# Performance work log

Hardware: AMD Instinct MI355X
Metric: run time of the kernel (lower is better)

The kernel has to match this reference:

```python
import jax, jax.numpy as jnp
import numpy as np

NUM_NODES = 10000
D = 128      # input_dim (embedding dim)
N = 64       # visit_code_num
V = 50       # visit_thresh (time steps)
B = 256      # batch
H = 384      # hidden_dim
L = 8        # levels
CH = H // L  # chunk_size
K = 10       # conv_size (sliding window / conv kernel)
OUT = 128    # output_dim
ND = N * D


def setup_inputs() -> dict:
    key = jax.random.key(0)
    ks = jax.random.split(key, 16)
    node_ids = jax.random.randint(ks[0], (B, V, N), 0, NUM_NODES + 1)
    edge_idx = jax.random.randint(ks[1], (2, 4), 0, 100)
    edge_attr = jax.random.normal(ks[2], (4, 1), jnp.float32)
    visit_times = jax.random.uniform(ks[3], (B, V), jnp.float32)
    visit_order = jax.random.randint(ks[4], (B, V), 0, V)
    attn_mask = jnp.zeros((B, V, N), dtype=bool)
    embed = jax.random.normal(ks[5], (NUM_NODES + 1, D), jnp.float32) * 0.02
    embed = embed.at[0].set(0.0)  # padding_idx=0
    G = 4 * H + 2 * L
    Wk = jax.random.normal(ks[6], (G, ND + 1), jnp.float32) * 0.01
    bk = jnp.zeros((G,), jnp.float32)
    Wr = jax.random.normal(ks[7], (G, H + 1), jnp.float32) * 0.05
    br = jnp.zeros((G,), jnp.float32)
    Ws = jax.random.normal(ks[8], (H // 6, H), jnp.float32) * 0.05
    bs = jnp.zeros((H // 6,), jnp.float32)
    Wrs = jax.random.normal(ks[9], (H, H // 6), jnp.float32) * 0.05
    brs = jnp.zeros((H,), jnp.float32)
    Wc = jax.random.normal(ks[10], (H, H, K), jnp.float32) * 0.02  # Conv1d weight [out,in,k]
    bc = jnp.zeros((H,), jnp.float32)
    Wo = jax.random.normal(ks[11], (OUT, H), jnp.float32) * 0.05
    bo = jnp.zeros((OUT,), jnp.float32)
    return dict(node_ids=node_ids, edge_idx=edge_idx, edge_attr=edge_attr,
                visit_times=visit_times, visit_order=visit_order, attn_mask=attn_mask,
                embed=embed, Wk=Wk, bk=bk, Wr=Wr, br=br, Ws=Ws, bs=bs,
                Wrs=Wrs, brs=brs, Wc=Wc, bc=bc, Wo=Wo, bo=bo)


def _cumax_l2r(z):
    return jnp.cumsum(jax.nn.softmax(z, -1), -1)


def _cumax_r2l(z):
    s = jax.nn.softmax(z, -1)
    return jnp.flip(jnp.cumsum(jnp.flip(s, -1), -1), -1)


def _forward(node_ids, attn_mask, visit_times, embed, Wk, bk, Wr, br,
             Ws, bs, Wrs, brs, Wc, bc, Wo, bo):
    b, v, n = node_ids.shape
    # gather(expand(embed), node_ids) == plain embedding lookup
    x = embed[node_ids].reshape(b, v, n * D)  # [B,V,ND]

    def step(carry, xt):
        c, h, tmp_h, tmp_dis = carry
        inp, interval = xt
        xi = jnp.concatenate([inp, interval[:, None]], -1)   # [B,ND+1]
        hi = jnp.concatenate([h, interval[:, None]], -1)     # [B,H+1]
        xout = xi @ Wk.T + bk + hi @ Wr.T + br               # [B,4H+2L]
        fm = _cumax_l2r(xout[:, :L])[:, :, None]             # [B,L,1]
        im = _cumax_r2l(xout[:, L:2 * L])[:, :, None]        # [B,L,1]
        g = xout[:, 2 * L:].reshape(b, 4 * L, CH)
        f = jax.nn.sigmoid(g[:, :L])
        i = jax.nn.sigmoid(g[:, L:2 * L])
        o = jax.nn.sigmoid(g[:, 2 * L:3 * L])
        cin = jnp.tanh(g[:, 3 * L:])
        cl = c.reshape(b, L, CH)
        ov = fm * im
        c_new = ov * (f * cl + i * cin) + (fm - ov) * cl + (im - ov) * cin
        h_new = (o * jnp.tanh(c_new)).reshape(b, H)
        c_new = c_new.reshape(b, H)
        cur_dist = 1.0 - jnp.mean(fm[:, :, 0], -1)           # [B]
        tmp_h = jnp.concatenate([tmp_h[1:], h_new[None]], 0)        # [K,B,H]
        tmp_dis = jnp.concatenate([tmp_dis[1:], cur_dist[None]], 0)  # [K,B]
        local_dis = jax.nn.softmax(jnp.cumsum(tmp_dis.T, 1), 1)     # [B,K]
        local_h = tmp_h.transpose(1, 2, 0) * local_dis[:, None, :]  # [B,H,K]
        theme = jnp.mean(local_h, -1)                               # [B,H]
        theme = jax.nn.sigmoid(jax.nn.relu(theme @ Ws.T + bs) @ Wrs.T + brs)
        conv = jnp.einsum('bhk,ohk->bo', local_h, Wc) + bc          # Conv1d, out len 1
        return (c_new, h_new, tmp_h, tmp_dis), (h_new, theme * conv)

    carry0 = (jnp.zeros((b, H), x.dtype), jnp.zeros((b, H), x.dtype),
              jnp.zeros((K, b, H), x.dtype), jnp.zeros((K, b), x.dtype))
    _, (origin_h, hs) = jax.lax.scan(step, carry0,
                                     (x.transpose(1, 0, 2), visit_times.T))
    rnn = (hs + origin_h).transpose(1, 0, 2)   # [B,V,H]
    output = rnn @ Wo.T + bo                   # [B,V,OUT]
    visit_mask = jnp.all(attn_mask, -1)        # [B,V] True = padded visit
    last = jnp.sum((~visit_mask).astype(jnp.int32), -1) - 1
    return output[jnp.arange(b), last]         # [B,OUT] logits


def reference(node_ids, edge_idx, edge_attr, visit_times, visit_order, attn_mask,
              embed, Wk, bk, Wr, br, Ws, bs, Wrs, brs, Wc, bc, Wo, bo):
    return _forward(node_ids, attn_mask, visit_times, embed, Wk, bk, Wr, br,
                    Ws, bs, Wrs, brs, Wc, bc, Wo, bo)
```

## Files before the change

kernel.cpp:

```cpp
#include <hip/hip_runtime.h>
#include <stdint.h>


typedef unsigned short u16;
typedef short bf16x8 __attribute__((ext_vector_type(8)));
typedef float f32x4 __attribute__((ext_vector_type(4)));

#define GLL(gp, lp)                                                            \
  __builtin_amdgcn_global_load_lds(                                            \
      (const __attribute__((address_space(1))) unsigned int*)(gp),             \
      (__attribute__((address_space(3))) unsigned int*)(lp), 16, 0, 0)

__device__ __forceinline__ float bf2f(u16 u) {
  union { unsigned int i; float f; } v;
  v.i = ((unsigned int)u) << 16;
  return v.f;
}
__device__ __forceinline__ u16 f2bf(float f) {
  union { float f; unsigned int i; } v;
  v.f = f;
  unsigned int r = (v.i + 0x7fffu + ((v.i >> 16) & 1u)) >> 16;
  return (u16)r;
}
__device__ __forceinline__ float ldf(const void* p, size_t i, int isbf) {
  return isbf ? bf2f(((const u16*)p)[i]) : ((const float*)p)[i];
}
__device__ __forceinline__ float sigf(float x) { return 1.f / (1.f + __expf(-x)); }
__device__ __forceinline__ float tanhf_(float x) {
  float cx = fminf(fmaxf(x, -15.f), 15.f);
  float e = __expf(2.f * cx);
  return (e - 1.f) / (e + 1.f);
}
__device__ __forceinline__ float dot8_bf(const u16* w, const float* lp) {
  uint4 wv = *(const uint4*)w;
  union { unsigned int u; float f; } a0, a1;
  float s;
  a0.u = wv.x << 16; a1.u = wv.x & 0xffff0000u;
  s = lp[0] * a0.f + lp[1] * a1.f;
  a0.u = wv.y << 16; a1.u = wv.y & 0xffff0000u;
  s += lp[2] * a0.f + lp[3] * a1.f;
  a0.u = wv.z << 16; a1.u = wv.z & 0xffff0000u;
  s += lp[4] * a0.f + lp[5] * a1.f;
  a0.u = wv.w << 16; a1.u = wv.w & 0xffff0000u;
  s += lp[6] * a0.f + lp[7] * a1.f;
  return s;
}

__device__ __forceinline__ int gperm(int gp) {
  if (gp < 16) return gp;
  int r = gp - 16;
  int q = r & 3, h = r >> 2;
  return 16 + q * 384 + h;
}

__global__ void k_detect(const unsigned int* __restrict__ emb_raw,
                         int* __restrict__ flag) {
  if (blockIdx.x == 0 && threadIdx.x == 0) {
    int cnt = 0;
    for (int i = 64; i < 128; ++i) {
      unsigned int u = emb_raw[i];
      unsigned int lo = u & 0xffffu;
      unsigned int ex = (lo >> 7) & 0xffu;
      if (lo != 0 && ex >= 100 && ex <= 126) ++cnt;
    }
    *flag = (cnt >= 32) ? 1 : 0;
  }
}

__global__ void k_cvt_emb(const void* __restrict__ src, u16* __restrict__ dst,
                          const int* __restrict__ flagp) {
  int isbf = *flagp;
  int n = 10001 * 128;
  int i = blockIdx.x * blockDim.x + threadIdx.x;
  int stride = gridDim.x * blockDim.x;
  for (; i < n; i += stride)
    dst[i] = isbf ? ((const u16*)src)[i] : f2bf(((const float*)src)[i]);
}

__global__ void k_repack_wk(const void* __restrict__ wk, u16* __restrict__ wkp,
                            const int* __restrict__ flagp) {
  int isbf = *flagp;
  size_t i = (size_t)blockIdx.x * blockDim.x + threadIdx.x;
  size_t total = (size_t)1664 * 8192;
  size_t stride = (size_t)gridDim.x * blockDim.x;
  for (; i < total; i += stride) {
    size_t gp = i >> 13, k = i & 8191;
    u16 v = (u16)0;
    if (gp < 1552) {
      int g = gperm((int)gp);
      v = f2bf(ldf(wk, (size_t)g * 8193 + k, isbf));
    }
    wkp[i] = v;
  }
}

__global__ void k_prep_wr2(const void* __restrict__ wr, const void* __restrict__ wk,
                           const void* __restrict__ bk, const void* __restrict__ br,
                           u16* __restrict__ wrP2, float* __restrict__ biasC,
                           float* __restrict__ wlC, const int* __restrict__ flagp) {
  int isbf = *flagp;
  int i0 = blockIdx.x * blockDim.x + threadIdx.x;
  int stride = gridDim.x * blockDim.x;
  for (int j = i0; j < 1552 * 384; j += stride) {
    int gp = j / 384, k = j - gp * 384;
    int g = gperm(gp);
    wrP2[j] = f2bf(ldf(wr, (size_t)g * 385 + k, isbf));
  }
  for (int gp = i0; gp < 1552; gp += stride) {
    int g = gperm(gp);
    biasC[gp] = ldf(bk, g, isbf) + ldf(br, g, isbf);
    wlC[gp] = ldf(wk, (size_t)g * 8193 + 8192, isbf) + ldf(wr, g * 385 + 384, isbf);
  }
}

__global__ void k_repack_wc(const void* __restrict__ wc, u16* __restrict__ wcp,
                            const int* __restrict__ flagp) {
  int isbf = *flagp;
  int i0 = blockIdx.x * blockDim.x + threadIdx.x;
  int stride = gridDim.x * blockDim.x;
  for (int j = i0; j < 384 * 3840; j += stride) {
    int o = j / 3840;
    int r = j - o * 3840;
    int k = r / 384;
    int h = r - k * 384;
    wcp[j] = f2bf(ldf(wc, (o * 384 + h) * 10 + k, isbf));
  }
}

__global__ void k_cvt_smalls(const void* vt, const void* Ws, const void* bs,
                             const void* Wrs, const void* brs, const void* bc,
                             const void* Wo, const void* bo,
                             float* __restrict__ dst, const int* __restrict__ flagp) {
  int isbf = *flagp;
  int i = blockIdx.x * blockDim.x + threadIdx.x;
  int stride = gridDim.x * blockDim.x;
  for (; i < 112064; i += stride) {
    float v;
    if (i < 12800) v = ldf(vt, i, isbf);
    else if (i < 37376) v = ldf(Ws, i - 12800, isbf);
    else if (i < 37440) v = ldf(bs, i - 37376, isbf);
    else if (i < 62016) v = ldf(Wrs, i - 37440, isbf);
    else if (i < 62400) v = ldf(brs, i - 62016, isbf);
    else if (i < 62784) v = ldf(bc, i - 62400, isbf);
    else if (i < 111936) v = ldf(Wo, i - 62784, isbf);
    else v = ldf(bo, i - 111936, isbf);
    dst[i] = v;
  }
}

__global__ void k_zero(float* __restrict__ p, int n) {
  int i = blockIdx.x * blockDim.x + threadIdx.x;
  int stride = gridDim.x * blockDim.x;
  for (; i < n; i += stride) p[i] = 0.f;
}

__global__ __launch_bounds__(256) void k_gemm_xk(
    const int* __restrict__ node_ids, const u16* __restrict__ embB,
    const u16* __restrict__ wkp, const float* __restrict__ vtF,
    const float* __restrict__ biasC, const float* __restrict__ wlC,
    u16* __restrict__ xkb) {
  __shared__ alignas(16) u16 As[128 * 64];
  __shared__ alignas(16) u16 Bs[128 * 64];
  __shared__ alignas(16) u16 idS[128 * 64];
  int tid = threadIdx.x;
  int lin = blockIdx.x;
  int xcd = lin & 7, slot = lin >> 3;
  int job = (xcd < 4) ? (xcd * 163 + slot) : (4 * 163 + (xcd - 4) * 162 + slot);
  int mb = job % 100, gb = job / 100;
  int m0 = mb * 128;
  int g0 = gb * 128;
  int tq = m0 >> 8, b0t = m0 & 255;
  int lane = tid & 63, w = tid >> 6;
  int wy = w >> 1, wx = w & 1;
  f32x4 acc[4][4];
#pragma unroll
  for (int i = 0; i < 4; ++i)
#pragma unroll
    for (int j = 0; j < 4; ++j) acc[i][j] = (f32x4){0.f, 0.f, 0.f, 0.f};

  {
    const int4* nb = (const int4*)(node_ids + ((size_t)b0t * 50 + tq) * 64);
    for (int i = tid; i < 2048; i += 256) {
      int row = i >> 4, c4 = i & 15;
      int4 v = nb[(size_t)row * 800 + c4];
      u16* d = idS + row * 64 + c4 * 4;
      d[0] = (u16)v.x; d[1] = (u16)v.y; d[2] = (u16)v.z; d[3] = (u16)v.w;
    }
  }

  int l15 = lane & 15, lq = lane >> 4;
  int lr = lane >> 3, lc = lane & 7;
  int swc = (lc ^ lr) * 8;
  int cRd = (lq ^ (l15 & 7)) * 8;

  for (int kt = 0; kt < 128; ++kt) {
    __syncthreads();
#pragma unroll
    for (int c = 0; c < 4; ++c) {
      int chunk = w * 4 + c;
      int r = chunk * 8 + lr;
      int id = (int)idS[r * 64 + (kt >> 1)];
      const u16* gp = embB + (size_t)id * 128 + (kt & 1) * 64 + swc;
      u16* lp = As + chunk * 512 + lane * 8;
      GLL(gp, lp);
    }
#pragma unroll
    for (int c = 0; c < 4; ++c) {
      int chunk = w * 4 + c;
      int r = chunk * 8 + lr;
      const u16* gp = wkp + (size_t)(g0 + r) * 8192 + (size_t)kt * 64 + swc;
      u16* lp = Bs + chunk * 512 + lane * 8;
      GLL(gp, lp);
    }
    __syncthreads();
    const u16* Ab = As + (wy * 64 + l15) * 64;
    const u16* Bb = Bs + (wx * 64 + l15) * 64;
#pragma unroll
    for (int ks = 0; ks < 2; ++ks) {
      int co = cRd ^ (ks * 32);
      bf16x8 av[4], bv[4];
#pragma unroll
      for (int i = 0; i < 4; ++i) av[i] = *(const bf16x8*)(Ab + i * 1024 + co);
#pragma unroll
      for (int j = 0; j < 4; ++j) bv[j] = *(const bf16x8*)(Bb + j * 1024 + co);
#pragma unroll
      for (int i = 0; i < 4; ++i)
#pragma unroll
        for (int j = 0; j < 4; ++j)
          acc[i][j] =
              __builtin_amdgcn_mfma_f32_16x16x32_bf16(av[i], bv[j], acc[i][j], 0, 0, 0);
    }
  }
  float vt[4][4];
#pragma unroll
  for (int i = 0; i < 4; ++i)
#pragma unroll
    for (int p = 0; p < 4; ++p)
      vt[i][p] = vtF[(size_t)(b0t + wy * 64 + i * 16 + lq * 4 + p) * 50 + tq];
#pragma unroll
  for (int j = 0; j < 4; ++j) {
    int gcol = g0 + wx * 64 + j * 16 + l15;
    if (gcol < 1552) {
      float bC = biasC[gcol], wC = wlC[gcol];
#pragma unroll
      for (int i = 0; i < 4; ++i)
#pragma unroll
        for (int p = 0; p < 4; ++p) {
          int row = wy * 64 + i * 16 + lq * 4 + p;
          xkb[(size_t)(m0 + row) * 1552 + gcol] =
              f2bf(acc[i][j][p] + bC + vt[i][p] * wC);
        }
    }
  }
}

__global__ __launch_bounds__(512) void k_step2(
    const u16* __restrict__ xkb,
    const u16* __restrict__ wrP2,
    float* __restrict__ hbuf,
    float* __restrict__ dbuf,
    const u16* __restrict__ hin,
    u16* __restrict__ hout,
    float* __restrict__ cst,
    int t) {
  __shared__ alignas(16) u16 hS[16 * 400];
  __shared__ alignas(16) float fmTile[16 * 17];
  __shared__ float fmS[16][8], imS[16][8];
  int tid = threadIdx.x;
  int gs = blockIdx.x, b0 = blockIdx.y * 16;
  int wv = tid >> 6, lane = tid & 63, l15 = lane & 15, lq = lane >> 4;

  int hmy = gs * 32 + wv * 4 + lq;
  int bmy = b0 + l15;

  uint2 xkg = *(const uint2*)(xkb + ((size_t)t * 256 + bmy) * 1552 + 16 +
                              gs * 128 + wv * 16 + lq * 4);
  uint4 xksm = (uint4){0u, 0u, 0u, 0u};
  if (tid < 32)
    xksm = *(const uint4*)(xkb + ((size_t)t * 256 + b0 + (tid & 15)) * 1552 +
                           ((tid < 16) ? 0 : 8));
  float cv = cst[(size_t)bmy * 384 + hmy];

  {
    const u16* hsrc = hin + (size_t)b0 * 384;
    for (int idx = tid; idx < 768; idx += 512) {
      int r = idx / 48, c = idx - r * 48;
      *(uint4*)(hS + r * 400 + c * 8) = *(const uint4*)(hsrc + r * 384 + c * 8);
    }
  }
  __syncthreads();

  bf16x8 hb[12];
#pragma unroll
  for (int ks = 0; ks < 12; ++ks)
    hb[ks] = *(const bf16x8*)(hS + l15 * 400 + ks * 32 + lq * 8);

  int gRow = 16 + gs * 128 + wv * 16 + l15;
  const u16* arow = wrP2 + (size_t)gRow * 384 + lq * 8;
  const u16* arow0 = wrP2 + (size_t)l15 * 384 + lq * 8;
  f32x4 accg = (f32x4){0.f, 0.f, 0.f, 0.f};
  f32x4 accf = (f32x4){0.f, 0.f, 0.f, 0.f};
#pragma unroll
  for (int ks = 0; ks < 12; ++ks) {
    bf16x8 ag = *(const bf16x8*)(arow + ks * 32);
    accg = __builtin_amdgcn_mfma_f32_16x16x32_bf16(ag, hb[ks], accg, 0, 0, 0);
    if (wv == 0) {
      bf16x8 a0 = *(const bf16x8*)(arow0 + ks * 32);
      accf = __builtin_amdgcn_mfma_f32_16x16x32_bf16(a0, hb[ks], accf, 0, 0, 0);
    }
  }
  if (wv == 0) {
#pragma unroll
    for (int p = 0; p < 4; ++p) fmTile[(lq * 4 + p) * 17 + l15] = accf[p];
  }
  __syncthreads();

  if (tid < 32) {
    int r = tid & 15;
    const u16* xs = (const u16*)&xksm;
    float z[8], m = -1e30f;
#pragma unroll
    for (int j = 0; j < 8; ++j) {
      int jj = (tid < 16) ? j : (8 + j);
      z[j] = fmTile[jj * 17 + r] + bf2f(xs[j]);
      m = fmaxf(m, z[j]);
    }
    float s = 0.f;
#pragma unroll
    for (int j = 0; j < 8; ++j) { z[j] = __expf(z[j] - m); s += z[j]; }
    float inv = 1.f / s;
    if (tid < 16) {
      float run = 0.f, fsum = 0.f;
#pragma unroll
      for (int j = 0; j < 8; ++j) { run += z[j] * inv; fmS[r][j] = run; fsum += run; }
      if (gs == 0) dbuf[(size_t)t * 256 + b0 + r] = 1.f - fsum * 0.125f;
    } else {
      float run = 0.f;
#pragma unroll
      for (int j = 7; j >= 0; --j) { run += z[j] * inv; imS[r][j] = run; }
    }
  }
  __syncthreads();

  {
    int lmy = hmy / 48;
    const u16* xg = (const u16*)&xkg;
    float x0 = accg[0] + bf2f(xg[0]);
    float x1 = accg[1] + bf2f(xg[1]);
    float x2 = accg[2] + bf2f(xg[2]);
    float x3 = accg[3] + bf2f(xg[3]);
    float fg = sigf(x0), ig = sigf(x1), og = sigf(x2), ci = tanhf_(x3);
    float fm = fmS[l15][lmy], im = imS[l15][lmy];
    float ov = fm * im;
    float cn = ov * (fg * cv + ig * ci) + (fm - ov) * cv + (im - ov) * ci;
    float hn = og * tanhf_(cn);
    cst[(size_t)bmy * 384 + hmy] = cn;
    hbuf[((size_t)t * 256 + bmy) * 384 + hmy] = hn;
    hout[(size_t)bmy * 384 + hmy] = f2bf(hn);
  }
}

__global__ __launch_bounds__(384) void k_final(
    const float* __restrict__ hbuf, const float* __restrict__ dbuf,
    const unsigned char* __restrict__ am, const float* __restrict__ smalls,
    const u16* __restrict__ wcp, float* __restrict__ out) {
  const float* WsF = smalls + 12800;
  const float* bsF = smalls + 37376;
  const float* WrsF = smalls + 37440;
  const float* brsF = smalls + 62016;
  const float* bcF = smalls + 62400;
  const float* WoF = smalls + 62784;
  const float* boF = smalls + 111936;
  __shared__ alignas(16) float lh2[10][384];
  __shared__ alignas(16) float ti[384];
  __shared__ alignas(16) float us[64];
  __shared__ alignas(16) float rnnS[384];
  __shared__ alignas(16) float hlastS[384];
  __shared__ float ldS[10];
  __shared__ int npad[50];
  __shared__ int lastS;
  int tid = threadIdx.x;
  int b = blockIdx.x;

  if (tid < 50) {
    const unsigned char* mr = am + ((size_t)b * 50 + tid) * 64;
    int all1 = 1;
    for (int q = 0; q < 64; ++q) all1 &= (mr[q] != 0);
    npad[tid] = all1 ? 0 : 1;
  }
  __syncthreads();
  if (tid == 0) {
    int c = 0;
    for (int v = 0; v < 50; ++v) c += npad[v];
    int lv = c - 1;
    int last = lv < 0 ? 0 : lv;
    lastS = last;
    float cum = 0.f, cv[10];
    for (int k = 0; k < 10; ++k) {
      int s = last - 9 + k;
      float dk = (s >= 0) ? dbuf[(size_t)s * 256 + b] : 0.f;
      cum += dk;
      cv[k] = cum;
    }
    float m = cv[0];
    for (int k = 1; k < 10; ++k) m = fmaxf(m, cv[k]);
    float ssum = 0.f, ee[10];
    for (int k = 0; k < 10; ++k) { ee[k] = __expf(cv[k] - m); ssum += ee[k]; }
    float inv = 1.f / ssum;
    for (int k = 0; k < 10; ++k) ldS[k] = ee[k] * inv;
  }
  __syncthreads();
  {
    int h = tid;
    int last = lastS;
    float ssum = 0.f;
    for (int k = 0; k < 10; ++k) {
      int s = last - 9 + k;
      float hv = (s >= 0) ? hbuf[((size_t)s * 256 + b) * 384 + h] : 0.f;
      float v = hv * ldS[k];
      lh2[k][h] = v;
      ssum += v;
    }
    ti[h] = ssum * 0.1f;
    hlastS[h] = hbuf[((size_t)last * 256 + b) * 384 + h];
  }
  __syncthreads();
  if (tid < 64) {
    float a = bsF[tid];
    const float* wr = WsF + (size_t)tid * 384;
    for (int h = 0; h < 384; ++h) a += wr[h] * ti[h];
    us[tid] = fmaxf(a, 0.f);
  }
  __syncthreads();
  {
    int o = tid;
    float th = brsF[o];
    const float* wr = WrsF + (size_t)o * 64;
    for (int k = 0; k < 64; ++k) th += wr[k] * us[k];
    th = sigf(th);
    float cacc = bcF[o];
    for (int k = 0; k < 10; ++k) {
      const u16* wrow = wcp + ((size_t)o * 10 + k) * 384;
      const float* lrow = lh2[k];
      for (int h8 = 0; h8 < 48; ++h8) cacc += dot8_bf(wrow + h8 * 8, lrow + h8 * 8);
    }
    rnnS[o] = th * cacc + hlastS[o];
  }
  __syncthreads();
  if (tid < 128) {
    float a = boF[tid];
    const float* wr = WoF + (size_t)tid * 384;
    for (int h = 0; h < 384; ++h) a += wr[h] * rnnS[h];
    out[(size_t)b * 128 + tid] = a;
  }
}

extern "C" void kernel_launch(void* const* d_in, const int* in_sizes, int n_in,
                              void* d_out, int out_size, void* d_ws, size_t ws_size,
                              hipStream_t stream) {
  const int* node_ids = (const int*)d_in[0];
  const void* vtR = d_in[3];
  const unsigned char* am = (const unsigned char*)d_in[5];
  const void* embR = d_in[6];
  const void* WkR = d_in[7];
  const void* bkR = d_in[8];
  const void* WrR = d_in[9];
  const void* brR = d_in[10];
  const void* WsR = d_in[11];
  const void* bsR = d_in[12];
  const void* WrsR = d_in[13];
  const void* brsR = d_in[14];
  const void* WcR = d_in[15];
  const void* bcR = d_in[16];
  const void* WoR = d_in[17];
  const void* boR = d_in[18];
  (void)in_sizes; (void)n_in; (void)out_size; (void)ws_size;

  char* ws = (char*)d_ws;
  size_t off = 0;
  auto alloc = [&](size_t bytes) {
    void* p = ws + off;
    off = (off + bytes + 255) & ~(size_t)255;
    return p;
  };
  int* flagp = (int*)alloc(4);
  u16* embB = (u16*)alloc((size_t)10001 * 128 * 2);
  u16* WkP = (u16*)alloc((size_t)1664 * 8192 * 2);
  u16* WrP2 = (u16*)alloc((size_t)1552 * 384 * 2);
  float* biasC = (float*)alloc(1552 * 4);
  float* wlC = (float*)alloc(1552 * 4);
  float* smalls = (float*)alloc((size_t)112064 * 4);
  u16* XKb = (u16*)alloc((size_t)12800 * 1552 * 2);
  u16* WcP = (u16*)alloc((size_t)384 * 3840 * 2);
  float* Hbuf = (float*)alloc((size_t)50 * 256 * 384 * 4);
  float* Dbuf = (float*)alloc((size_t)50 * 256 * 4);
  u16* Hx = (u16*)alloc((size_t)2 * 256 * 384 * 2);
  float* Cst = (float*)alloc((size_t)256 * 384 * 4);

  k_detect<<<dim3(1), dim3(64), 0, stream>>>((const unsigned int*)embR, flagp);
  k_cvt_emb<<<dim3(1024), dim3(256), 0, stream>>>(embR, embB, flagp);
  k_repack_wk<<<dim3(2048), dim3(256), 0, stream>>>(WkR, WkP, flagp);
  k_prep_wr2<<<dim3(512), dim3(256), 0, stream>>>(WrR, WkR, bkR, brR, WrP2, biasC,
                                                  wlC, flagp);
  k_repack_wc<<<dim3(512), dim3(256), 0, stream>>>(WcR, WcP, flagp);
  k_cvt_smalls<<<dim3(128), dim3(256), 0, stream>>>(vtR, WsR, bsR, WrsR, brsR,
                                                    bcR, WoR, boR, smalls, flagp);
  k_zero<<<dim3(96), dim3(256), 0, stream>>>((float*)Hx, 98304);
  k_zero<<<dim3(96), dim3(256), 0, stream>>>(Cst, 98304);

  k_gemm_xk<<<dim3(1300), dim3(256), 0, stream>>>(node_ids, embB, WkP, smalls,
                                                  biasC, wlC, XKb);

  for (int t = 0; t < 50; ++t) {
    const u16* hin = Hx + (size_t)(t & 1) * (256 * 384);
    u16* hout = Hx + (size_t)((t + 1) & 1) * (256 * 384);
    k_step2<<<dim3(12, 16), dim3(512), 0, stream>>>(XKb, WrP2, Hbuf, Dbuf, hin,
                                                    hout, Cst, t);
  }

  k_final<<<dim3(256), dim3(384), 0, stream>>>(Hbuf, Dbuf, am, smalls, WcP,
                                               (float*)d_out);
}
```

Before: 1.128 ms.

## Fuse 50 recurrent step launches into one persistent kernel with per-group barriers

Replaces 50 separate per-timestep launches with a single persistent kernel of 192 blocks. Each block keeps its recurrent weight slice in LDS and its cell state in registers. Blocks exchange bf16 hidden state through global memory and sync per batch group with an atomic counter spin barrier. This removes launch overhead and repeated weight and cell-state reloads, but relies on all 192 blocks being co-resident and on relaxed atomics for visibility. It also pads the id tile in shared memory to reduce bank conflicts in the gather GEMM.

Measured after the change: 993.2 us. -11.9%, faster.

```diff
diff --git a/kernel.cpp b/kernel.cpp
--- a/kernel.cpp
+++ b/kernel.cpp
@@ -161,7 +161,7 @@
     u16* __restrict__ xkb) {
   __shared__ alignas(16) u16 As[128 * 64];
   __shared__ alignas(16) u16 Bs[128 * 64];
-  __shared__ alignas(16) u16 idS[128 * 64];
+  __shared__ alignas(16) u16 idS[128 * 66];
   int tid = threadIdx.x;
   int lin = blockIdx.x;
   int xcd = lin & 7, slot = lin >> 3;
@@ -183,7 +183,7 @@
     for (int i = tid; i < 2048; i += 256) {
       int row = i >> 4, c4 = i & 15;
       int4 v = nb[(size_t)row * 800 + c4];
-      u16* d = idS + row * 64 + c4 * 4;
+      u16* d = idS + row * 66 + c4 * 4;
       d[0] = (u16)v.x; d[1] = (u16)v.y; d[2] = (u16)v.z; d[3] = (u16)v.w;
     }
   }
@@ -199,7 +199,7 @@
     for (int c = 0; c < 4; ++c) {
       int chunk = w * 4 + c;
       int r = chunk * 8 + lr;
-      int id = (int)idS[r * 64 + (kt >> 1)];
+      int id = (int)idS[r * 66 + (kt >> 1)];
       const u16* gp = embB + (size_t)id * 128 + (kt & 1) * 64 + swc;
       u16* lp = As + chunk * 512 + lane * 8;
       GLL(gp, lp);
@@ -254,109 +254,153 @@
   }
 }
 
-__global__ __launch_bounds__(512) void k_step2(
+__global__ __launch_bounds__(512) void k_scan5(
     const u16* __restrict__ xkb,
     const u16* __restrict__ wrP2,
     float* __restrict__ hbuf,
     float* __restrict__ dbuf,
-    const u16* __restrict__ hin,
-    u16* __restrict__ hout,
-    float* __restrict__ cst,
-    int t) {
-  __shared__ alignas(16) u16 hS[16 * 400];
+    unsigned int* __restrict__ hx,
+    int* __restrict__ barCnt) {
+  __shared__ alignas(16) u16 WrS[144 * 392];
+  __shared__ alignas(16) u16 hS[16 * 392];
   __shared__ alignas(16) float fmTile[16 * 17];
   __shared__ float fmS[16][8], imS[16][8];
+
   int tid = threadIdx.x;
-  int gs = blockIdx.x, b0 = blockIdx.y * 16;
+  int L = blockIdx.x;
+  int xcd = L & 7, kk = L >> 3;
+  int hi = (kk >= 12) ? 1 : 0;
+  int bg = (xcd << 1) | hi;
+  int gs = kk - 12 * hi;
+  int b0 = bg * 16;
   int wv = tid >> 6, lane = tid & 63, l15 = lane & 15, lq = lane >> 4;
 
+  for (int idx = tid; idx < 144 * 48; idx += 512) {
+    int r = idx / 48, c = idx - r * 48;
+    int gr = (r < 16) ? r : (16 + gs * 128 + (r - 16));
+    *(uint4*)(WrS + r * 392 + c * 8) =
+        *(const uint4*)(wrP2 + (size_t)gr * 384 + c * 8);
+  }
+
   int hmy = gs * 32 + wv * 4 + lq;
+  int lmy = hmy / 48;
   int bmy = b0 + l15;
-
-  uint2 xkg = *(const uint2*)(xkb + ((size_t)t * 256 + bmy) * 1552 + 16 +
-                              gs * 128 + wv * 16 + lq * 4);
-  uint4 xksm = (uint4){0u, 0u, 0u, 0u};
-  if (tid < 32)
-    xksm = *(const uint4*)(xkb + ((size_t)t * 256 + b0 + (tid & 15)) * 1552 +
-                           ((tid < 16) ? 0 : 8));
-  float cv = cst[(size_t)bmy * 384 + hmy];
-
-  {
-    const u16* hsrc = hin + (size_t)b0 * 384;
-    for (int idx = tid; idx < 768; idx += 512) {
-      int r = idx / 48, c = idx - r * 48;
-      *(uint4*)(hS + r * 400 + c * 8) = *(const uint4*)(hsrc + r * 384 + c * 8);
-    }
-  }
+  float creg = 0.f;
+
+  const u16* arow_g = WrS + (16 + wv * 16 + l15) * 392 + lq * 8;
+  const u16* arow_f = WrS + l15 * 392 + lq * 8;
+  const u16* brow = hS + l15 * 392 + lq * 8;
   __syncthreads();
 
-  bf16x8 hb[12];
-#pragma unroll
-  for (int ks = 0; ks < 12; ++ks)
-    hb[ks] = *(const bf16x8*)(hS + l15 * 400 + ks * 32 + lq * 8);
-
-  int gRow = 16 + gs * 128 + wv * 16 + l15;
-  const u16* arow = wrP2 + (size_t)gRow * 384 + lq * 8;
-  const u16* arow0 = wrP2 + (size_t)l15 * 384 + lq * 8;
-  f32x4 accg = (f32x4){0.f, 0.f, 0.f, 0.f};
-  f32x4 accf = (f32x4){0.f, 0.f, 0.f, 0.f};
-#pragma unroll
-  for (int ks = 0; ks < 12; ++ks) {
-    bf16x8 ag = *(const bf16x8*)(arow + ks * 32);
-    accg = __builtin_amdgcn_mfma_f32_16x16x32_bf16(ag, hb[ks], accg, 0, 0, 0);
+  for (int t = 0; t < 50; ++t) {
+    uint2 xkg = *(const uint2*)(xkb + ((size_t)t * 256 + bmy) * 1552 + 16 +
+                                gs * 128 + wv * 16 + lq * 4);
+    uint4 xksm = (uint4){0u, 0u, 0u, 0u};
+    if (tid < 32)
+      xksm = *(const uint4*)(xkb + ((size_t)t * 256 + b0 + (tid & 15)) * 1552 +
+                             ((tid < 16) ? 0 : 8));
+
+    {
+      const unsigned int* hxin = hx + (size_t)(t & 1) * 49152 + (size_t)b0 * 192;
+#pragma unroll
+      for (int k2 = 0; k2 < 6; ++k2) {
+        int j = tid + k2 * 512;
+        int r = j / 192, c = j - r * 192;
+        unsigned int v = __hip_atomic_load(&hxin[r * 192 + c], __ATOMIC_RELAXED,
+                                           __HIP_MEMORY_SCOPE_AGENT);
+        *(unsigned int*)((char*)hS + r * 784 + c * 4) = v;
+      }
+    }
+    __syncthreads();
+
+    bf16x8 hb[12];
+#pragma unroll
+    for (int ks = 0; ks < 12; ++ks)
+      hb[ks] = *(const bf16x8*)(brow + ks * 32);
+
+    f32x4 accg = (f32x4){0.f, 0.f, 0.f, 0.f};
+    f32x4 accf = (f32x4){0.f, 0.f, 0.f, 0.f};
+#pragma unroll
+    for (int ks = 0; ks < 12; ++ks) {
+      bf16x8 ag = *(const bf16x8*)(arow_g + ks * 32);
+      accg = __builtin_amdgcn_mfma_f32_16x16x32_bf16(ag, hb[ks], accg, 0, 0, 0);
+      if (wv == 0) {
+        bf16x8 a0 = *(const bf16x8*)(arow_f + ks * 32);
+        accf = __builtin_amdgcn_mfma_f32_16x16x32_bf16(a0, hb[ks], accf, 0, 0, 0);
+      }
+    }
     if (wv == 0) {
-      bf16x8 a0 = *(const bf16x8*)(arow0 + ks * 32);
-      accf = __builtin_amdgcn_mfma_f32_16x16x32_bf16(a0, hb[ks], accf, 0, 0, 0);
-    }
-  }
-  if (wv == 0) {
-#pragma unroll
-    for (int p = 0; p < 4; ++p) fmTile[(lq * 4 + p) * 17 + l15] = accf[p];
-  }
-  __syncthreads();
-
-  if (tid < 32) {
-    int r = tid & 15;
-    const u16* xs = (const u16*)&xksm;
-    float z[8], m = -1e30f;
-#pragma unroll
-    for (int j = 0; j < 8; ++j) {
-      int jj = (tid < 16) ? j : (8 + j);
-      z[j] = fmTile[jj * 17 + r] + bf2f(xs[j]);
-      m = fmaxf(m, z[j]);
-    }
-    float s = 0.f;
-#pragma unroll
-    for (int j = 0; j < 8; ++j) { z[j] = __expf(z[j] - m); s += z[j]; }
-    float inv = 1.f / s;
-    if (tid < 16) {
-      float run = 0.f, fsum = 0.f;
-#pragma unroll
-      for (int j = 0; j < 8; ++j) { run += z[j] * inv; fmS[r][j] = run; fsum += run; }
-      if (gs == 0) dbuf[(size_t)t * 256 + b0 + r] = 1.f - fsum * 0.125f;
-    } else {
-      float run = 0.f;
-#pragma unroll
-      for (int j = 7; j >= 0; --j) { run += z[j] * inv; imS[r][j] = run; }
-    }
-  }
-  __syncthreads();
-
-  {
-    int lmy = hmy / 48;
-    const u16* xg = (const u16*)&xkg;
-    float x0 = accg[0] + bf2f(xg[0]);
-    float x1 = accg[1] + bf2f(xg[1]);
-    float x2 = accg[2] + bf2f(xg[2]);
-    float x3 = accg[3] + bf2f(xg[3]);
-    float fg = sigf(x0), ig = sigf(x1), og = sigf(x2), ci = tanhf_(x3);
-    float fm = fmS[l15][lmy], im = imS[l15][lmy];
-    float ov = fm * im;
-    float cn = ov * (fg * cv + ig * ci) + (fm - ov) * cv + (im - ov) * ci;
-    float hn = og * tanhf_(cn);
-    cst[(size_t)bmy * 384 + hmy] = cn;
-    hbuf[((size_t)t * 256 + bmy) * 384 + hmy] = hn;
-    hout[(size_t)bmy * 384 + hmy] = f2bf(hn);
+#pragma unroll
+      for (int p = 0; p < 4; ++p) fmTile[(lq * 4 + p) * 17 + l15] = accf[p];
+    }
+    __syncthreads();
+
+    if (tid < 32) {
+      int r = tid & 15;
+      const u16* xs = (const u16*)&xksm;
+      float z[8], m = -1e30f;
+#pragma unroll
+      for (int j = 0; j < 8; ++j) {
+        int jj = (tid < 16) ? j : (8 + j);
+        z[j] = fmTile[jj * 17 + r] + bf2f(xs[j]);
+        m = fmaxf(m, z[j]);
+      }
+      float s = 0.f;
+#pragma unroll
+      for (int j = 0; j < 8; ++j) { z[j] = __expf(z[j] - m); s += z[j]; }
+      float inv = 1.f / s;
+      if (tid < 16) {
+        float run = 0.f, fsum = 0.f;
+#pragma unroll
+        for (int j = 0; j < 8; ++j) { run += z[j] * inv; fmS[r][j] = run; fsum += run; }
+        if (gs == 0) dbuf[(size_t)t * 256 + b0 + r] = 1.f - fsum * 0.125f;
+      } else {
+        float run = 0.f;
+#pragma unroll
+        for (int j = 7; j >= 0; --j) { run += z[j] * inv; imS[r][j] = run; }
+      }
+    }
+    __syncthreads();
+
+    {
+      const u16* xg = (const u16*)&xkg;
+      float x0 = accg[0] + bf2f(xg[0]);
+      float x1 = accg[1] + bf2f(xg[1]);
+      float x2 = accg[2] + bf2f(xg[2]);
+      float x3 = accg[3] + bf2f(xg[3]);
+      float fg = sigf(x0), ig = sigf(x1), og = sigf(x2), ci = tanhf_(x3);
+      float fm = fmS[l15][lmy], im = imS[l15][lmy];
+      float ov = fm * im;
+      float cn = ov * (fg * creg + ig * ci) + (fm - ov) * creg + (im - ov) * ci;
+      float hn = og * tanhf_(cn);
+      creg = cn;
+      hbuf[((size_t)t * 256 + bmy) * 384 + hmy] = hn;
+      if (t != 49) {
+        unsigned int v = (unsigned int)f2bf(hn);
+        unsigned int up = __shfl_down(v, 16);
+        if ((lq & 1) == 0) {
+          unsigned int packed = v | (up << 16);
+          __hip_atomic_store(
+              &hx[(size_t)((t + 1) & 1) * 49152 + (size_t)bmy * 192 + gs * 16 +
+                  wv * 2 + (lq >> 1)],
+              packed, __ATOMIC_RELAXED, __HIP_MEMORY_SCOPE_AGENT);
+        }
+      }
+    }
+
+    if (t != 49) {
+      asm volatile("s_waitcnt vmcnt(0)" ::: "memory");
+      __syncthreads();
+      if (tid == 0) {
+        __hip_atomic_fetch_add(&barCnt[bg], 1, __ATOMIC_RELAXED,
+                               __HIP_MEMORY_SCOPE_AGENT);
+        while (__hip_atomic_load(&barCnt[bg], __ATOMIC_RELAXED,
+                                 __HIP_MEMORY_SCOPE_AGENT) < 12 * (t + 1)) {
+          __builtin_amdgcn_s_sleep(1);
+        }
+      }
+      __syncthreads();
+    }
   }
 }
 
@@ -494,8 +538,8 @@
   u16* WcP = (u16*)alloc((size_t)384 * 3840 * 2);
   float* Hbuf = (float*)alloc((size_t)50 * 256 * 384 * 4);
   float* Dbuf = (float*)alloc((size_t)50 * 256 * 4);
-  u16* Hx = (u16*)alloc((size_t)2 * 256 * 384 * 2);
-  float* Cst = (float*)alloc((size_t)256 * 384 * 4);
+  unsigned int* Hx = (unsigned int*)alloc((size_t)2 * 256 * 192 * 4);
+  int* BarCnt = (int*)alloc(16 * 4);
 
   k_detect<<<dim3(1), dim3(64), 0, stream>>>((const unsigned int*)embR, flagp);
   k_cvt_emb<<<dim3(1024), dim3(256), 0, stream>>>(embR, embB, flagp);
@@ -506,17 +550,12 @@
   k_cvt_smalls<<<dim3(128), dim3(256), 0, stream>>>(vtR, WsR, bsR, WrsR, brsR,
                                                     bcR, WoR, boR, smalls, flagp);
   k_zero<<<dim3(96), dim3(256), 0, stream>>>((float*)Hx, 98304);
-  k_zero<<<dim3(96), dim3(256), 0, stream>>>(Cst, 98304);
+  k_zero<<<dim3(1), dim3(64), 0, stream>>>((float*)BarCnt, 16);
 
   k_gemm_xk<<<dim3(1300), dim3(256), 0, stream>>>(node_ids, embB, WkP, smalls,
                                                   biasC, wlC, XKb);
 
-  for (int t = 0; t < 50; ++t) {
-    const u16* hin = Hx + (size_t)(t & 1) * (256 * 384);
-    u16* hout = Hx + (size_t)((t + 1) & 1) * (256 * 384);
-    k_step2<<<dim3(12, 16), dim3(512), 0, stream>>>(XKb, WrP2, Hbuf, Dbuf, hin,
-                                                    hout, Cst, t);
-  }
+  k_scan5<<<dim3(192), dim3(512), 0, stream>>>(XKb, WrP2, Hbuf, Dbuf, Hx, BarCnt);
 
   k_final<<<dim3(256), dim3(384), 0, stream>>>(Hbuf, Dbuf, am, smalls, WcP,
                                                (float*)d_out);
```
